# Kernel tuning notes

Measured on AMD Instinct MI355X. Metric: run time of the kernel, lower is better.

The kernel has to match this reference:

```python
import jax, jax.numpy as jnp
import numpy as np

B, N_NODE, N_EDGE_TYPES, L, D = 8, 2000, 2, 8, 64
NNZ = 32000


def spmm(vals, rows, cols, state):
    """Sparse (N_NODE x E*N_NODE) @ dense state [E*N_NODE, L, D] -> [N_NODE, L, D].
    vals/rows/cols: [NNZ] COO entries."""
    msgs = state[cols] * vals[:, None, None]          # [NNZ, L, D]
    return jax.ops.segment_sum(msgs, rows, num_segments=N_NODE)


def setup_inputs() -> dict:
    key = jax.random.key(0)
    ks = jax.random.split(key, 12)
    EN = N_EDGE_TYPES * N_NODE
    scale = 1.0 / np.sqrt(3 * D).astype(np.float32)
    return {
        "state_in": jax.random.normal(ks[0], (B, EN, L, D), jnp.float32),
        "state_out": jax.random.normal(ks[1], (B, EN, L, D), jnp.float32),
        "state_cur": jax.random.normal(ks[2], (B, N_NODE, L, D), jnp.float32),
        "A_vals": jax.random.uniform(ks[3], (B, 2, NNZ), jnp.float32),
        "A_rows": jax.random.randint(ks[4], (B, 2, NNZ), 0, N_NODE, jnp.int32),
        "A_cols": jax.random.randint(ks[5], (B, 2, NNZ), 0, EN, jnp.int32),
        "W_r": jax.random.normal(ks[6], (D, 3 * D), jnp.float32) * scale,
        "b_r": jnp.zeros((D,), jnp.float32),
        "W_z": jax.random.normal(ks[7], (D, 3 * D), jnp.float32) * scale,
        "b_z": jnp.zeros((D,), jnp.float32),
        "W_h": jax.random.normal(ks[8], (D, 3 * D), jnp.float32) * scale,
        "b_h": jnp.zeros((D,), jnp.float32),
    }


def reference(state_in, state_out, state_cur, A_vals, A_rows, A_cols,
              W_r, b_r, W_z, b_z, W_h, b_h):
    spmm_b = jax.vmap(spmm)
    # batched sparse adjacency matmul for in- and out-edges
    a_in = spmm_b(A_vals[:, 0], A_rows[:, 0], A_cols[:, 0], state_in)    # [B,N,L,D]
    a_out = spmm_b(A_vals[:, 1], A_rows[:, 1], A_cols[:, 1], state_out)  # [B,N,L,D]
    a = jnp.concatenate([a_in, a_out, state_cur], axis=3)                # [B,N,L,3D]
    r = jax.nn.sigmoid(jnp.einsum('bnli,oi->bnlo', a, W_r) + b_r)
    z = jax.nn.sigmoid(jnp.einsum('bnli,oi->bnlo', a, W_z) + b_z)
    joined = jnp.concatenate([a_in, a_out, r * state_cur], axis=3)
    h_hat = jnp.tanh(jnp.einsum('bnli,oi->bnlo', joined, W_h) + b_h)
    return (1.0 - z) * state_cur + z * h_hat
```

## Files before the change

### kernel.cpp

```cpp
#include <hip/hip_runtime.h>
#include <math.h>

#define B_    8
#define N_    2000
#define ET_   2
#define L_    8
#define D_    64
#define NNZ_  32000
#define EN_   4000
#define LD_   512
#define SEGS_ 16
#define SEGSTR_ 2001
#define TOTE_ 512000
#define ROWS_ 128000
#define STHALF_ 16384000
#define CAP_  48

typedef __attribute__((ext_vector_type(8))) short short8;
typedef __attribute__((ext_vector_type(4))) float f32x4;

__device__ __forceinline__ ushort bf(float x) {
    unsigned u = __float_as_uint(x);
    unsigned r = (u + 0x7FFFu + ((u >> 16) & 1u)) >> 16;
    return (ushort)r;
}

__device__ __forceinline__ float fast_tanh(float x) {
    float e = __expf(-2.f * fabsf(x));
    float t = (1.f - e) / (1.f + e);
    return (x < 0.f) ? -t : t;
}

__global__ __launch_bounds__(256) void prep_a_kernel(
    const float* __restrict__ s_in, const float* __restrict__ s_out,
    ushort* __restrict__ st_bf,
    const int* __restrict__ rows, const float* __restrict__ vals,
    const int* __restrict__ cols, int* __restrict__ cursor,
    uint2* __restrict__ bucket,
    const float* __restrict__ Wr, const float* __restrict__ Wz,
    const float* __restrict__ Wh, ushort* __restrict__ Wbf) {
    int bid = blockIdx.x;
    int tid = threadIdx.x;
    if (bid < 2048) {
        int gid = bid * 256 + tid;
        f32x4 v[16];
#pragma unroll
        for (int k = 0; k < 8; ++k) {
            int c = gid + k * 524288;
            if (c < 4096000) {
                size_t idx = (size_t)c * 8;
                const f32x4* src;
                if (idx < (size_t)STHALF_) src = (const f32x4*)(s_in + idx);
                else                       src = (const f32x4*)(s_out + (idx - STHALF_));
                v[2 * k]     = __builtin_nontemporal_load(src);
                v[2 * k + 1] = __builtin_nontemporal_load(src + 1);
            }
        }
#pragma unroll
        for (int k = 0; k < 8; ++k) {
            int c = gid + k * 524288;
            if (c < 4096000) {
                size_t idx = (size_t)c * 8;
                f32x4 v0 = v[2 * k], v1 = v[2 * k + 1];
                union { ushort u[8]; uint4 q; } pk;
                pk.u[0] = bf(v0.x); pk.u[1] = bf(v0.y); pk.u[2] = bf(v0.z); pk.u[3] = bf(v0.w);
                pk.u[4] = bf(v1.x); pk.u[5] = bf(v1.y); pk.u[6] = bf(v1.z); pk.u[7] = bf(v1.w);
                *(uint4*)(st_bf + idx) = pk.q;
            }
        }
    } else if (bid < 4048) {
        int idx = (bid - 2048) * 256 + tid;
        int seg = idx / NNZ_;
        int row = rows[idx];
        int slot = seg * N_ + row;
        int pos = atomicAdd(&cursor[slot], 1);
        if (pos < CAP_) {
            uint2 e;
            e.x = __float_as_uint(vals[idx]);
            e.y = (unsigned)cols[idx];
            bucket[(size_t)slot * CAP_ + pos] = e;
        }
    } else {
        int cid = (bid - 4048) * 256 + tid;
        int row = cid / 24, c0 = (cid % 24) * 8;
        const float* src = (row < 64) ? (Wr + row * 192)
                         : (row < 128) ? (Wz + (row - 64) * 192)
                                       : (Wh + (row - 128) * 192);
        float4 v0 = *(const float4*)(src + c0);
        float4 v1 = *(const float4*)(src + c0 + 4);
        union { ushort u[8]; uint4 v; } pk;
        pk.u[0] = bf(v0.x); pk.u[1] = bf(v0.y); pk.u[2] = bf(v0.z); pk.u[3] = bf(v0.w);
        pk.u[4] = bf(v1.x); pk.u[5] = bf(v1.y); pk.u[6] = bf(v1.z); pk.u[7] = bf(v1.w);
        *(uint4*)(Wbf + row * 192 + c0) = pk.v;
    }
}

__global__ __launch_bounds__(256) void gather_a_kernel(
    const ushort* __restrict__ st_bf, const uint2* __restrict__ bucket,
    const int* __restrict__ cursor, ushort* __restrict__ abuf) {
    int xcd = blockIdx.x & 7;
    int s = blockIdx.x >> 3;
    int half = (s >= 500) ? 1 : 0;
    int seg = xcd * 2 + half;
    int row = (s - half * 500) * 4 + (threadIdx.x >> 6);
    int lane = threadIdx.x & 63;
    int b = seg >> 1, t = seg & 1;
    const ushort* stp = st_bf + (size_t)t * STHALF_ + (size_t)b * (EN_ * LD_) + lane * 8;
    int slot = seg * N_ + row;
    int cnt = cursor[slot];
    if (cnt > CAP_) cnt = CAP_;
    const uint2* ec = bucket + (size_t)slot * CAP_;
    float acc[8];
#pragma unroll
    for (int k = 0; k < 8; ++k) acc[k] = 0.f;

    int j = 0;
    for (; j + 4 <= cnt; j += 4) {
        uint2 e0 = ec[j];
        uint2 e1 = ec[j + 1];
        uint2 e2 = ec[j + 2];
        uint2 e3 = ec[j + 3];
        uint4 x0 = *(const uint4*)(stp + (size_t)e0.y * LD_);
        uint4 x1 = *(const uint4*)(stp + (size_t)e1.y * LD_);
        uint4 x2 = *(const uint4*)(stp + (size_t)e2.y * LD_);
        uint4 x3 = *(const uint4*)(stp + (size_t)e3.y * LD_);
        float v0 = __uint_as_float(e0.x), v1 = __uint_as_float(e1.x);
        float v2 = __uint_as_float(e2.x), v3 = __uint_as_float(e3.x);
        uint xs0[4] = {x0.x, x0.y, x0.z, x0.w};
        uint xs1[4] = {x1.x, x1.y, x1.z, x1.w};
        uint xs2[4] = {x2.x, x2.y, x2.z, x2.w};
        uint xs3[4] = {x3.x, x3.y, x3.z, x3.w};
#pragma unroll
        for (int k = 0; k < 4; ++k) {
            acc[2 * k]     += v0 * __uint_as_float(xs0[k] << 16);
            acc[2 * k + 1] += v0 * __uint_as_float(xs0[k] & 0xFFFF0000u);
            acc[2 * k]     += v1 * __uint_as_float(xs1[k] << 16);
            acc[2 * k + 1] += v1 * __uint_as_float(xs1[k] & 0xFFFF0000u);
            acc[2 * k]     += v2 * __uint_as_float(xs2[k] << 16);
            acc[2 * k + 1] += v2 * __uint_as_float(xs2[k] & 0xFFFF0000u);
            acc[2 * k]     += v3 * __uint_as_float(xs3[k] << 16);
            acc[2 * k + 1] += v3 * __uint_as_float(xs3[k] & 0xFFFF0000u);
        }
    }
    for (; j < cnt; ++j) {
        uint2 e = ec[j];
        float v = __uint_as_float(e.x);
        uint4 x = *(const uint4*)(stp + (size_t)e.y * LD_);
        uint xs[4] = {x.x, x.y, x.z, x.w};
#pragma unroll
        for (int k = 0; k < 4; ++k) {
            acc[2 * k]     += v * __uint_as_float(xs[k] << 16);
            acc[2 * k + 1] += v * __uint_as_float(xs[k] & 0xFFFF0000u);
        }
    }

    union { ushort u[8]; uint4 v; } pk;
#pragma unroll
    for (int k = 0; k < 8; ++k) pk.u[k] = bf(acc[k]);
    ushort* dst = abuf + ((size_t)((t * B_ + b) * N_ + row)) * LD_ + lane * 8;
    *(uint4*)dst = pk.v;
}

__global__ __launch_bounds__(256) void prep_kernel(
    const float* __restrict__ s_in, const float* __restrict__ s_out,
    ushort* __restrict__ st_bf,
    const int* __restrict__ rows, int* __restrict__ ptr,
    const float* __restrict__ Wr, const float* __restrict__ Wz,
    const float* __restrict__ Wh, ushort* __restrict__ Wbf) {
    int bid = blockIdx.x;
    int tid = threadIdx.x;
    if (bid < 2048) {
        int gid = bid * 256 + tid;
        f32x4 v[16];
#pragma unroll
        for (int k = 0; k < 8; ++k) {
            int c = gid + k * 524288;
            if (c < 4096000) {
                size_t idx = (size_t)c * 8;
                const f32x4* src;
                if (idx < (size_t)STHALF_) src = (const f32x4*)(s_in + idx);
                else                       src = (const f32x4*)(s_out + (idx - STHALF_));
                v[2 * k]     = __builtin_nontemporal_load(src);
                v[2 * k + 1] = __builtin_nontemporal_load(src + 1);
            }
        }
#pragma unroll
        for (int k = 0; k < 8; ++k) {
            int c = gid + k * 524288;
            if (c < 4096000) {
                size_t idx = (size_t)c * 8;
                f32x4 v0 = v[2 * k], v1 = v[2 * k + 1];
                union { ushort u[8]; uint4 q; } pk;
                pk.u[0] = bf(v0.x); pk.u[1] = bf(v0.y); pk.u[2] = bf(v0.z); pk.u[3] = bf(v0.w);
                pk.u[4] = bf(v1.x); pk.u[5] = bf(v1.y); pk.u[6] = bf(v1.z); pk.u[7] = bf(v1.w);
                *(uint4*)(st_bf + idx) = pk.q;
            }
        }
    } else if (bid < 4048) {
        int idx = (bid - 2048) * 256 + tid;
        int seg = idx / NNZ_;
        int row = rows[idx];
        atomicAdd(&ptr[seg * SEGSTR_ + row + 1], 1);
    } else {
        int cid = (bid - 4048) * 256 + tid;
        int row = cid / 24, c0 = (cid % 24) * 8;
        const float* src = (row < 64) ? (Wr + row * 192)
                         : (row < 128) ? (Wz + (row - 64) * 192)
                                       : (Wh + (row - 128) * 192);
        float4 v0 = *(const float4*)(src + c0);
        float4 v1 = *(const float4*)(src + c0 + 4);
        union { ushort u[8]; uint4 v; } pk;
        pk.u[0] = bf(v0.x); pk.u[1] = bf(v0.y); pk.u[2] = bf(v0.z); pk.u[3] = bf(v0.w);
        pk.u[4] = bf(v1.x); pk.u[5] = bf(v1.y); pk.u[6] = bf(v1.z); pk.u[7] = bf(v1.w);
        *(uint4*)(Wbf + row * 192 + c0) = pk.v;
    }
}

__global__ void scan_kernel(int* __restrict__ ptr, int* __restrict__ cursor) {
    int seg = blockIdx.x;
    int* p = ptr + seg * SEGSTR_;
    int* c = cursor + seg * SEGSTR_;
    __shared__ int totals[256];
    int t = threadIdx.x;
    int v[8];
    int run = 0;
    int base = t * 8;
#pragma unroll
    for (int k = 0; k < 8; ++k) {
        int i = base + k;
        int x = (i < SEGSTR_) ? p[i] : 0;
        run += x;
        v[k] = run;
    }
    totals[t] = run;
    __syncthreads();
    if (t == 0) {
        int r = 0;
        for (int i = 0; i < 256; ++i) { int tmp = totals[i]; totals[i] = r; r += tmp; }
    }
    __syncthreads();
    int off = totals[t];
#pragma unroll
    for (int k = 0; k < 8; ++k) {
        int i = base + k;
        if (i < SEGSTR_) {
            int val = off + v[k];
            p[i] = val;
            c[i] = val;
        }
    }
}

__global__ void fill_kernel(const int* __restrict__ rows, const float* __restrict__ vals,
                            const int* __restrict__ cols, int* __restrict__ cursor,
                            uint2* __restrict__ ec_s) {
    int idx = blockIdx.x * 256 + threadIdx.x;
    int seg = idx / NNZ_;
    int row = rows[idx];
    int pos = atomicAdd(&cursor[seg * SEGSTR_ + row], 1);
    uint2 e;
    e.x = __float_as_uint(vals[idx]);
    e.y = (unsigned)cols[idx];
    ec_s[seg * NNZ_ + pos] = e;
}

__global__ __launch_bounds__(256) void gather_bf_kernel(
    const ushort* __restrict__ st_bf, const uint2* __restrict__ ec_s,
    const int* __restrict__ ptr, ushort* __restrict__ abuf) {
    int xcd = blockIdx.x & 7;
    int s = blockIdx.x >> 3;
    int half = (s >= 500) ? 1 : 0;
    int seg = xcd * 2 + half;
    int row = (s - half * 500) * 4 + (threadIdx.x >> 6);
    int lane = threadIdx.x & 63;
    int b = seg >> 1, t = seg & 1;
    const ushort* stp = st_bf + (size_t)t * STHALF_ + (size_t)b * (EN_ * LD_) + lane * 8;
    int s0 = ptr[seg * SEGSTR_ + row];
    int s1 = ptr[seg * SEGSTR_ + row + 1];
    const uint2* ec = ec_s + seg * NNZ_;
    float acc[8];
#pragma unroll
    for (int k = 0; k < 8; ++k) acc[k] = 0.f;
    int j = s0;
    for (; j + 4 <= s1; j += 4) {
        uint2 e0 = ec[j];
        uint2 e1 = ec[j + 1];
        uint2 e2 = ec[j + 2];
        uint2 e3 = ec[j + 3];
        uint4 x0 = *(const uint4*)(stp + (size_t)e0.y * LD_);
        uint4 x1 = *(const uint4*)(stp + (size_t)e1.y * LD_);
        uint4 x2 = *(const uint4*)(stp + (size_t)e2.y * LD_);
        uint4 x3 = *(const uint4*)(stp + (size_t)e3.y * LD_);
        float v0 = __uint_as_float(e0.x), v1 = __uint_as_float(e1.x);
        float v2 = __uint_as_float(e2.x), v3 = __uint_as_float(e3.x);
        uint xs0[4] = {x0.x, x0.y, x0.z, x0.w};
        uint xs1[4] = {x1.x, x1.y, x1.z, x1.w};
        uint xs2[4] = {x2.x, x2.y, x2.z, x2.w};
        uint xs3[4] = {x3.x, x3.y, x3.z, x3.w};
#pragma unroll
        for (int k = 0; k < 4; ++k) {
            acc[2 * k]     += v0 * __uint_as_float(xs0[k] << 16);
            acc[2 * k + 1] += v0 * __uint_as_float(xs0[k] & 0xFFFF0000u);
            acc[2 * k]     += v1 * __uint_as_float(xs1[k] << 16);
            acc[2 * k + 1] += v1 * __uint_as_float(xs1[k] & 0xFFFF0000u);
            acc[2 * k]     += v2 * __uint_as_float(xs2[k] << 16);
            acc[2 * k + 1] += v2 * __uint_as_float(xs2[k] & 0xFFFF0000u);
            acc[2 * k]     += v3 * __uint_as_float(xs3[k] << 16);
            acc[2 * k + 1] += v3 * __uint_as_float(xs3[k] & 0xFFFF0000u);
        }
    }
    for (; j < s1; ++j) {
        uint2 e = ec[j];
        float v = __uint_as_float(e.x);
        uint4 x = *(const uint4*)(stp + (size_t)e.y * LD_);
        uint xs[4] = {x.x, x.y, x.z, x.w};
#pragma unroll
        for (int k = 0; k < 4; ++k) {
            acc[2 * k]     += v * __uint_as_float(xs[k] << 16);
            acc[2 * k + 1] += v * __uint_as_float(xs[k] & 0xFFFF0000u);
        }
    }
    union { ushort u[8]; uint4 v; } pk;
#pragma unroll
    for (int k = 0; k < 8; ++k) pk.u[k] = bf(acc[k]);
    ushort* dst = abuf + ((size_t)((t * B_ + b) * N_ + row)) * LD_ + lane * 8;
    *(uint4*)dst = pk.v;
}

__global__ __launch_bounds__(256) void gather_f32_kernel(
    const float* __restrict__ state_in, const float* __restrict__ state_out,
    const uint2* __restrict__ ec_s, const int* __restrict__ ptr,
    ushort* __restrict__ abuf) {
    int xcd = blockIdx.x & 7;
    int s = blockIdx.x >> 3;
    int half = (s >= 500) ? 1 : 0;
    int seg = xcd * 2 + half;
    int row = (s - half * 500) * 4 + (threadIdx.x >> 6);
    int lane = threadIdx.x & 63;
    int b = seg >> 1, t = seg & 1;
    const float* st = (t ? state_out : state_in) + (size_t)b * (EN_ * LD_) + lane * 8;
    int s0 = ptr[seg * SEGSTR_ + row];
    int s1 = ptr[seg * SEGSTR_ + row + 1];
    const uint2* ec = ec_s + seg * NNZ_;
    float4 a0 = make_float4(0.f, 0.f, 0.f, 0.f);
    float4 a1 = make_float4(0.f, 0.f, 0.f, 0.f);
    for (int j = s0; j < s1; ++j) {
        uint2 e = ec[j];
        float v = __uint_as_float(e.x);
        const float* src = st + (size_t)e.y * LD_;
        float4 x0 = *(const float4*)src;
        float4 x1 = *(const float4*)(src + 4);
        a0.x += v * x0.x; a0.y += v * x0.y; a0.z += v * x0.z; a0.w += v * x0.w;
        a1.x += v * x1.x; a1.y += v * x1.y; a1.z += v * x1.z; a1.w += v * x1.w;
    }
    union { ushort u[8]; uint4 v; } pk;
    pk.u[0] = bf(a0.x); pk.u[1] = bf(a0.y); pk.u[2] = bf(a0.z); pk.u[3] = bf(a0.w);
    pk.u[4] = bf(a1.x); pk.u[5] = bf(a1.y); pk.u[6] = bf(a1.z); pk.u[7] = bf(a1.w);
    ushort* dst = abuf + ((size_t)((t * B_ + b) * N_ + row)) * LD_ + lane * 8;
    *(uint4*)dst = pk.v;
}

__global__ void wprep_kernel(const float* __restrict__ Wr, const float* __restrict__ Wz,
                             const float* __restrict__ Wh, ushort* __restrict__ Wbf) {
    int cid = blockIdx.x * 256 + threadIdx.x;
    if (cid >= 4608) return;
    int row = cid / 24, c0 = (cid % 24) * 8;
    const float* src = (row < 64) ? (Wr + row * 192)
                     : (row < 128) ? (Wz + (row - 64) * 192)
                                   : (Wh + (row - 128) * 192);
    float4 v0 = *(const float4*)(src + c0);
    float4 v1 = *(const float4*)(src + c0 + 4);
    union { ushort u[8]; uint4 v; } pk;
    pk.u[0] = bf(v0.x); pk.u[1] = bf(v0.y); pk.u[2] = bf(v0.z); pk.u[3] = bf(v0.w);
    pk.u[4] = bf(v1.x); pk.u[5] = bf(v1.y); pk.u[6] = bf(v1.z); pk.u[7] = bf(v1.w);
    *(uint4*)(Wbf + row * 192 + c0) = pk.v;
}

__global__ void hist_kernel(const int* __restrict__ rows, int* __restrict__ ptr) {
    int idx = blockIdx.x * 256 + threadIdx.x;
    int seg = idx / NNZ_;
    int row = rows[idx];
    atomicAdd(&ptr[seg * SEGSTR_ + row + 1], 1);
}

__global__ __launch_bounds__(256) void gru_kernel(
    const ushort* __restrict__ abuf, const float* __restrict__ state_cur,
    const ushort* __restrict__ Wbf,
    const float* __restrict__ br, const float* __restrict__ bz, const float* __restrict__ bh,
    float* __restrict__ out) {
    __shared__ ushort wsh[64][196];
    __shared__ ushort rcur[64][72];
    int tid = threadIdx.x;
    int wave = tid >> 6, lane = tid & 63;
    int b = blockIdx.x & 7;
    int tile = blockIdx.x >> 3;
    int R0 = b * (N_ * L_) + tile * 64;
    int g = lane >> 4;
    int oc = lane & 15;
    int arow = wave * 16 + oc;
    int rbase = wave * 16 + g * 4;

    {
        const uint4* srcw = (const uint4*)(Wbf);
#pragma unroll
        for (int j = 0; j < 6; ++j) {
            int i = tid + j * 256;
            int row = i / 24, c4 = i - row * 24;
            *(uint4*)&wsh[row][c4 * 8] = srcw[i];
        }
    }

    short8 afr[6];
    {
        const ushort* pin  = abuf + (size_t)(R0 + arow) * 64 + g * 8;
        const ushort* pout = pin + (size_t)ROWS_ * 64;
        afr[0] = *(const short8*)(pin);
        afr[1] = *(const short8*)(pin + 32);
        afr[2] = *(const short8*)(pout);
        afr[3] = *(const short8*)(pout + 32);
        const float* pc = state_cur + (size_t)(R0 + arow) * 64 + g * 8;
        float4 u0 = *(const float4*)(pc);
        float4 u1 = *(const float4*)(pc + 4);
        float4 u2 = *(const float4*)(pc + 32);
        float4 u3 = *(const float4*)(pc + 36);
        short8 t4, t5;
        t4[0] = (short)bf(u0.x); t4[1] = (short)bf(u0.y); t4[2] = (short)bf(u0.z); t4[3] = (short)bf(u0.w);
        t4[4] = (short)bf(u1.x); t4[5] = (short)bf(u1.y); t4[6] = (short)bf(u1.z); t4[7] = (short)bf(u1.w);
        t5[0] = (short)bf(u2.x); t5[1] = (short)bf(u2.y); t5[2] = (short)bf(u2.z); t5[3] = (short)bf(u2.w);
        t5[4] = (short)bf(u3.x); t5[5] = (short)bf(u3.y); t5[6] = (short)bf(u3.z); t5[7] = (short)bf(u3.w);
        afr[4] = t4; afr[5] = t5;
    }

    float curv[4][4];
#pragma unroll
    for (int ct = 0; ct < 4; ++ct)
#pragma unroll
        for (int q = 0; q < 4; ++q)
            curv[ct][q] = state_cur[(size_t)(R0 + rbase + q) * 64 + ct * 16 + oc];

    __syncthreads();

    f32x4 accR[4];
#pragma unroll
    for (int ct = 0; ct < 4; ++ct) accR[ct] = (f32x4)(0.f);
#pragma unroll
    for (int ct = 0; ct < 4; ++ct) {
#pragma unroll
        for (int s = 0; s < 6; ++s) {
            short8 bfr = *(const short8*)&wsh[ct * 16 + oc][s * 32 + g * 8];
            accR[ct] = __builtin_amdgcn_mfma_f32_16x16x32_bf16(afr[s], bfr, accR[ct], 0, 0, 0);
        }
    }
    __syncthreads();

    {
        const uint4* srcw = (const uint4*)(Wbf + 64 * 192);
#pragma unroll
        for (int j = 0; j < 6; ++j) {
            int i = tid + j * 256;
            int row = i / 24, c4 = i - row * 24;
            *(uint4*)&wsh[row][c4 * 8] = srcw[i];
        }
    }
#pragma unroll
    for (int ct = 0; ct < 4; ++ct) {
        float brl = br[ct * 16 + oc];
#pragma unroll
        for (int q = 0; q < 4; ++q) {
            float rg = 1.f / (1.f + __expf(-(accR[ct][q] + brl)));
            rcur[rbase + q][ct * 16 + oc] = bf(rg * curv[ct][q]);
        }
    }
    __syncthreads();

    f32x4 accZ[4];
#pragma unroll
    for (int ct = 0; ct < 4; ++ct) accZ[ct] = (f32x4)(0.f);
#pragma unroll
    for (int ct = 0; ct < 4; ++ct) {
#pragma unroll
        for (int s = 0; s < 6; ++s) {
            short8 bfr = *(const short8*)&wsh[ct * 16 + oc][s * 32 + g * 8];
            accZ[ct] = __builtin_amdgcn_mfma_f32_16x16x32_bf16(afr[s], bfr, accZ[ct], 0, 0, 0);
        }
    }
    __syncthreads();

    {
        const uint4* srcw = (const uint4*)(Wbf + 128 * 192);
#pragma unroll
        for (int j = 0; j < 6; ++j) {
            int i = tid + j * 256;
            int row = i / 24, c4 = i - row * 24;
            *(uint4*)&wsh[row][c4 * 8] = srcw[i];
        }
    }
    __syncthreads();

    short8 afh4 = *(const short8*)&rcur[arow][g * 8];
    short8 afh5 = *(const short8*)&rcur[arow][32 + g * 8];
    f32x4 accH[4];
#pragma unroll
    for (int ct = 0; ct < 4; ++ct) accH[ct] = (f32x4)(0.f);
#pragma unroll
    for (int ct = 0; ct < 4; ++ct) {
#pragma unroll
        for (int s = 0; s < 6; ++s) {
            short8 bfr = *(const short8*)&wsh[ct * 16 + oc][s * 32 + g * 8];
            short8 a = (s < 4) ? afr[s] : (s == 4 ? afh4 : afh5);
            accH[ct] = __builtin_amdgcn_mfma_f32_16x16x32_bf16(a, bfr, accH[ct], 0, 0, 0);
        }
    }

#pragma unroll
    for (int ct = 0; ct < 4; ++ct) {
        float bzl = bz[ct * 16 + oc];
        float bhl = bh[ct * 16 + oc];
#pragma unroll
        for (int q = 0; q < 4; ++q) {
            float z = 1.f / (1.f + __expf(-(accZ[ct][q] + bzl)));
            float hh = fast_tanh(accH[ct][q] + bhl);
            out[(size_t)(R0 + rbase + q) * 64 + ct * 16 + oc] =
                (1.f - z) * curv[ct][q] + z * hh;
        }
    }
}

extern "C" void kernel_launch(void* const* d_in, const int* in_sizes, int n_in,
                              void* d_out, int out_size, void* d_ws, size_t ws_size,
                              hipStream_t stream) {
    const float* state_in  = (const float*)d_in[0];
    const float* state_out = (const float*)d_in[1];
    const float* state_cur = (const float*)d_in[2];
    const float* A_vals    = (const float*)d_in[3];
    const int*   A_rows    = (const int*)d_in[4];
    const int*   A_cols    = (const int*)d_in[5];
    const float* W_r = (const float*)d_in[6];
    const float* b_r = (const float*)d_in[7];
    const float* W_z = (const float*)d_in[8];
    const float* b_z = (const float*)d_in[9];
    const float* W_h = (const float*)d_in[10];
    const float* b_h = (const float*)d_in[11];
    float* out = (float*)d_out;

    char* p0 = (char*)d_ws;
    ushort* abuf = (ushort*)p0;
    ushort* Wbf  = (ushort*)(p0 + (size_t)2 * ROWS_ * 64 * 2);
    char* p = p0 + (size_t)2 * ROWS_ * 64 * 2 + 36864 * 2;

    int*    cursorA = (int*)p;
    uint2*  bucket  = (uint2*)(p + (size_t)SEGS_ * N_ * 4);
    ushort* st_bfA  = (ushort*)(p + (size_t)SEGS_ * N_ * 4 + (size_t)SEGS_ * N_ * CAP_ * 8);
    size_t needA = ((char*)(st_bfA + (size_t)2 * STHALF_)) - p0;

    int*    ptrB    = (int*)p;
    int*    cursorB = (int*)(p + 32016 * 4);
    uint2*  ec_s    = (uint2*)(p + 32016 * 8);
    ushort* st_bfB  = (ushort*)(p + 32016 * 8 + (size_t)SEGS_ * NNZ_ * 8);
    size_t needB = ((char*)(st_bfB + (size_t)2 * STHALF_)) - p0;

    if (ws_size >= needA) {
        hipMemsetAsync(cursorA, 0, (size_t)SEGS_ * N_ * 4, stream);
        prep_a_kernel<<<4066, 256, 0, stream>>>(state_in, state_out, st_bfA,
                                                A_rows, A_vals, A_cols, cursorA, bucket,
                                                W_r, W_z, W_h, Wbf);
        gather_a_kernel<<<SEGS_ * N_ / 4, 256, 0, stream>>>(st_bfA, bucket, cursorA, abuf);
    } else if (ws_size >= needB) {
        hipMemsetAsync(ptrB, 0, 32016 * sizeof(int), stream);
        prep_kernel<<<4066, 256, 0, stream>>>(state_in, state_out, st_bfB,
                                              A_rows, ptrB, W_r, W_z, W_h, Wbf);
        scan_kernel<<<SEGS_, 256, 0, stream>>>(ptrB, cursorB);
        fill_kernel<<<TOTE_ / 256, 256, 0, stream>>>(A_rows, A_vals, A_cols, cursorB, ec_s);
        gather_bf_kernel<<<SEGS_ * N_ / 4, 256, 0, stream>>>(st_bfB, ec_s, ptrB, abuf);
    } else {
        hipMemsetAsync(ptrB, 0, 32016 * sizeof(int), stream);
        wprep_kernel<<<18, 256, 0, stream>>>(W_r, W_z, W_h, Wbf);
        hist_kernel<<<TOTE_ / 256, 256, 0, stream>>>(A_rows, ptrB);
        scan_kernel<<<SEGS_, 256, 0, stream>>>(ptrB, cursorB);
        fill_kernel<<<TOTE_ / 256, 256, 0, stream>>>(A_rows, A_vals, A_cols, cursorB, ec_s);
        gather_f32_kernel<<<SEGS_ * N_ / 4, 256, 0, stream>>>(state_in, state_out,
                                                              ec_s, ptrB, abuf);
    }
    gru_kernel<<<ROWS_ / 64, 256, 0, stream>>>(abuf, state_cur, Wbf,
                                               b_r, b_z, b_h, out);
}
```

Baseline: 124.9 us.

## Process two 64-row tiles per GRU block and drop nontemporal state loads

The GRU kernel now handles 128 rows per block as two 64-row sub-tiles. Each weight fragment read from LDS feeds two MFMAs, and the per-gate weight staging to shared memory is amortised over twice the rows, with half as many blocks launched. Separately, the bf16 conversion of state_in/state_out now uses ordinary loads instead of nontemporal loads, which may keep the converted data in cache for the later gather. The cost is higher register pressure and fewer blocks, which could lower occupancy.

```diff
diff --git a/kernel.cpp b/kernel.cpp
--- a/kernel.cpp
+++ b/kernel.cpp
@@ -52,8 +52,8 @@
                 const f32x4* src;
                 if (idx < (size_t)STHALF_) src = (const f32x4*)(s_in + idx);
                 else                       src = (const f32x4*)(s_out + (idx - STHALF_));
-                v[2 * k]     = __builtin_nontemporal_load(src);
-                v[2 * k + 1] = __builtin_nontemporal_load(src + 1);
+                v[2 * k]     = src[0];
+                v[2 * k + 1] = src[1];
             }
         }
 #pragma unroll
@@ -180,8 +180,8 @@
                 const f32x4* src;
                 if (idx < (size_t)STHALF_) src = (const f32x4*)(s_in + idx);
                 else                       src = (const f32x4*)(s_out + (idx - STHALF_));
-                v[2 * k]     = __builtin_nontemporal_load(src);
-                v[2 * k + 1] = __builtin_nontemporal_load(src + 1);
+                v[2 * k]     = src[0];
+                v[2 * k + 1] = src[1];
             }
         }
 #pragma unroll
@@ -389,12 +389,12 @@
     const float* __restrict__ br, const float* __restrict__ bz, const float* __restrict__ bh,
     float* __restrict__ out) {
     __shared__ ushort wsh[64][196];
-    __shared__ ushort rcur[64][72];
+    __shared__ ushort rcur[128][72];
     int tid = threadIdx.x;
     int wave = tid >> 6, lane = tid & 63;
     int b = blockIdx.x & 7;
-    int tile = blockIdx.x >> 3;
-    int R0 = b * (N_ * L_) + tile * 64;
+    int tile2 = blockIdx.x >> 3;
+    int Rb = b * (N_ * L_) + tile2 * 128;
     int g = lane >> 4;
     int oc = lane & 15;
     int arow = wave * 16 + oc;
@@ -410,14 +410,17 @@
         }
     }
 
-    short8 afr[6];
-    {
+    short8 afr0[6], afr1[6];
+    float curv0[4][4], curv1[4][4];
+#pragma unroll
+    for (int u = 0; u < 2; ++u) {
+        int R0 = Rb + u * 64;
         const ushort* pin  = abuf + (size_t)(R0 + arow) * 64 + g * 8;
         const ushort* pout = pin + (size_t)ROWS_ * 64;
-        afr[0] = *(const short8*)(pin);
-        afr[1] = *(const short8*)(pin + 32);
-        afr[2] = *(const short8*)(pout);
-        afr[3] = *(const short8*)(pout + 32);
+        short8 a0 = *(const short8*)(pin);
+        short8 a1 = *(const short8*)(pin + 32);
+        short8 a2 = *(const short8*)(pout);
+        short8 a3 = *(const short8*)(pout + 32);
         const float* pc = state_cur + (size_t)(R0 + arow) * 64 + g * 8;
         float4 u0 = *(const float4*)(pc);
         float4 u1 = *(const float4*)(pc + 4);
@@ -428,27 +431,28 @@
         t4[4] = (short)bf(u1.x); t4[5] = (short)bf(u1.y); t4[6] = (short)bf(u1.z); t4[7] = (short)bf(u1.w);
         t5[0] = (short)bf(u2.x); t5[1] = (short)bf(u2.y); t5[2] = (short)bf(u2.z); t5[3] = (short)bf(u2.w);
         t5[4] = (short)bf(u3.x); t5[5] = (short)bf(u3.y); t5[6] = (short)bf(u3.z); t5[7] = (short)bf(u3.w);
-        afr[4] = t4; afr[5] = t5;
-    }
-
-    float curv[4][4];
-#pragma unroll
-    for (int ct = 0; ct < 4; ++ct)
-#pragma unroll
-        for (int q = 0; q < 4; ++q)
-            curv[ct][q] = state_cur[(size_t)(R0 + rbase + q) * 64 + ct * 16 + oc];
+        short8* afr = u ? afr1 : afr0;
+        afr[0] = a0; afr[1] = a1; afr[2] = a2; afr[3] = a3; afr[4] = t4; afr[5] = t5;
+        float (*cv)[4] = u ? curv1 : curv0;
+#pragma unroll
+        for (int ct = 0; ct < 4; ++ct)
+#pragma unroll
+            for (int q = 0; q < 4; ++q)
+                cv[ct][q] = state_cur[(size_t)(R0 + rbase + q) * 64 + ct * 16 + oc];
+    }
 
     __syncthreads();
 
-    f32x4 accR[4];
-#pragma unroll
-    for (int ct = 0; ct < 4; ++ct) accR[ct] = (f32x4)(0.f);
+    f32x4 accR0[4], accR1[4];
+#pragma unroll
+    for (int ct = 0; ct < 4; ++ct) { accR0[ct] = (f32x4)(0.f); accR1[ct] = (f32x4)(0.f); }
 #pragma unroll
     for (int ct = 0; ct < 4; ++ct) {
 #pragma unroll
         for (int s = 0; s < 6; ++s) {
             short8 bfr = *(const short8*)&wsh[ct * 16 + oc][s * 32 + g * 8];
-            accR[ct] = __builtin_amdgcn_mfma_f32_16x16x32_bf16(afr[s], bfr, accR[ct], 0, 0, 0);
+            accR0[ct] = __builtin_amdgcn_mfma_f32_16x16x32_bf16(afr0[s], bfr, accR0[ct], 0, 0, 0);
+            accR1[ct] = __builtin_amdgcn_mfma_f32_16x16x32_bf16(afr1[s], bfr, accR1[ct], 0, 0, 0);
         }
     }
     __syncthreads();
@@ -467,21 +471,24 @@
         float brl = br[ct * 16 + oc];
 #pragma unroll
         for (int q = 0; q < 4; ++q) {
-            float rg = 1.f / (1.f + __expf(-(accR[ct][q] + brl)));
-            rcur[rbase + q][ct * 16 + oc] = bf(rg * curv[ct][q]);
+            float rg0 = 1.f / (1.f + __expf(-(accR0[ct][q] + brl)));
+            rcur[rbase + q][ct * 16 + oc] = bf(rg0 * curv0[ct][q]);
+            float rg1 = 1.f / (1.f + __expf(-(accR1[ct][q] + brl)));
+            rcur[64 + rbase + q][ct * 16 + oc] = bf(rg1 * curv1[ct][q]);
         }
     }
     __syncthreads();
 
-    f32x4 accZ[4];
-#pragma unroll
-    for (int ct = 0; ct < 4; ++ct) accZ[ct] = (f32x4)(0.f);
+    f32x4 accZ0[4], accZ1[4];
+#pragma unroll
+    for (int ct = 0; ct < 4; ++ct) { accZ0[ct] = (f32x4)(0.f); accZ1[ct] = (f32x4)(0.f); }
 #pragma unroll
     for (int ct = 0; ct < 4; ++ct) {
 #pragma unroll
         for (int s = 0; s < 6; ++s) {
             short8 bfr = *(const short8*)&wsh[ct * 16 + oc][s * 32 + g * 8];
-            accZ[ct] = __builtin_amdgcn_mfma_f32_16x16x32_bf16(afr[s], bfr, accZ[ct], 0, 0, 0);
+            accZ0[ct] = __builtin_amdgcn_mfma_f32_16x16x32_bf16(afr0[s], bfr, accZ0[ct], 0, 0, 0);
+            accZ1[ct] = __builtin_amdgcn_mfma_f32_16x16x32_bf16(afr1[s], bfr, accZ1[ct], 0, 0, 0);
         }
     }
     __syncthreads();
@@ -497,18 +504,22 @@
     }
     __syncthreads();
 
-    short8 afh4 = *(const short8*)&rcur[arow][g * 8];
-    short8 afh5 = *(const short8*)&rcur[arow][32 + g * 8];
-    f32x4 accH[4];
-#pragma unroll
-    for (int ct = 0; ct < 4; ++ct) accH[ct] = (f32x4)(0.f);
+    short8 afh40 = *(const short8*)&rcur[arow][g * 8];
+    short8 afh50 = *(const short8*)&rcur[arow][32 + g * 8];
+    short8 afh41 = *(const short8*)&rcur[64 + arow][g * 8];
+    short8 afh51 = *(const short8*)&rcur[64 + arow][32 + g * 8];
+    f32x4 accH0[4], accH1[4];
+#pragma unroll
+    for (int ct = 0; ct < 4; ++ct) { accH0[ct] = (f32x4)(0.f); accH1[ct] = (f32x4)(0.f); }
 #pragma unroll
     for (int ct = 0; ct < 4; ++ct) {
 #pragma unroll
         for (int s = 0; s < 6; ++s) {
             short8 bfr = *(const short8*)&wsh[ct * 16 + oc][s * 32 + g * 8];
-            short8 a = (s < 4) ? afr[s] : (s == 4 ? afh4 : afh5);
-            accH[ct] = __builtin_amdgcn_mfma_f32_16x16x32_bf16(a, bfr, accH[ct], 0, 0, 0);
+            short8 a0 = (s < 4) ? afr0[s] : (s == 4 ? afh40 : afh50);
+            accH0[ct] = __builtin_amdgcn_mfma_f32_16x16x32_bf16(a0, bfr, accH0[ct], 0, 0, 0);
+            short8 a1 = (s < 4) ? afr1[s] : (s == 4 ? afh41 : afh51);
+            accH1[ct] = __builtin_amdgcn_mfma_f32_16x16x32_bf16(a1, bfr, accH1[ct], 0, 0, 0);
         }
     }
 
@@ -518,10 +529,14 @@
         float bhl = bh[ct * 16 + oc];
 #pragma unroll
         for (int q = 0; q < 4; ++q) {
-            float z = 1.f / (1.f + __expf(-(accZ[ct][q] + bzl)));
-            float hh = fast_tanh(accH[ct][q] + bhl);
-            out[(size_t)(R0 + rbase + q) * 64 + ct * 16 + oc] =
-                (1.f - z) * curv[ct][q] + z * hh;
+            float z0 = 1.f / (1.f + __expf(-(accZ0[ct][q] + bzl)));
+            float h0 = fast_tanh(accH0[ct][q] + bhl);
+            out[(size_t)(Rb + rbase + q) * 64 + ct * 16 + oc] =
+                (1.f - z0) * curv0[ct][q] + z0 * h0;
+            float z1 = 1.f / (1.f + __expf(-(accZ1[ct][q] + bzl)));
+            float h1 = fast_tanh(accH1[ct][q] + bhl);
+            out[(size_t)(Rb + 64 + rbase + q) * 64 + ct * 16 + oc] =
+                (1.f - z1) * curv1[ct][q] + z1 * h1;
         }
     }
 }
@@ -581,6 +596,6 @@
         gather_f32_kernel<<<SEGS_ * N_ / 4, 256, 0, stream>>>(state_in, state_out,
                                                               ec_s, ptrB, abuf);
     }
-    gru_kernel<<<ROWS_ / 64, 256, 0, stream>>>(abuf, state_cur, Wbf,
-                                               b_r, b_z, b_h, out);
-}
+    gru_kernel<<<ROWS_ / 128, 256, 0, stream>>>(abuf, state_cur, Wbf,
+                                                b_r, b_z, b_h, out);
+}
```

After: 131.9 us. 5.6% more time.
